# Kernel optimization log

Measured on AMD Instinct MI355X. Metric: run time of the kernel, lower is better.

The kernel has to match this reference:

```python
import jax, jax.numpy as jnp
import numpy as np

REG_COEF = 0.001


def setup_inputs() -> dict:
    key = jax.random.key(0)
    k1, k2, k3, k4 = jax.random.split(key, 4)
    B, K, d = 8192, 1024, 64
    q = jax.random.normal(k1, (B, d), dtype=jnp.float32)
    c = jax.random.normal(k2, (K, d), dtype=jnp.float32)
    # positive bandwidths, as produced by adjust_bandwidth (1/(2*rho^2))
    bandwidth = jax.random.uniform(k3, (K,), dtype=jnp.float32, minval=0.1, maxval=1.0)
    g_inv_c = jax.random.normal(k4, (K, d, d), dtype=jnp.float32)
    return {"q": q, "c": c, "bandwidth": bandwidth, "g_inv_c": g_inv_c}


def reference(q, c, bandwidth, g_inv_c):
    # squared euclidean distances: ||q-c||^2, computed via the expanded form
    sq_q = jnp.sum(q * q, axis=-1, keepdims=True)           # (B,1)
    sq_c = jnp.sum(c * c, axis=-1)                          # (K,)
    d2 = jnp.maximum(sq_q + sq_c[None, :] - 2.0 * (q @ c.T), 0.0)  # (B,K)
    weights = jnp.exp(-bandwidth[None, :] * d2)             # (B,K)
    g_inv = jnp.einsum('bk,kij->bij', weights, g_inv_c)     # (B,d,d)
    d = q.shape[-1]
    g_inv = g_inv + REG_COEF * jnp.eye(d, dtype=q.dtype)[None, :, :]
    return g_inv
```

## Files before the change

kernel.cpp:

```cpp
#include <hip/hip_runtime.h>
#include <hip/hip_bf16.h>

typedef __attribute__((ext_vector_type(8))) short bf16x8;
typedef __attribute__((ext_vector_type(4))) float f32x4;

#define Bsz 8192
#define Ksz 1024
#define Dsz 64
#define Nsz 4096

__device__ __forceinline__ void async_load16(const void* g, void* lds) {
    __builtin_amdgcn_global_load_lds(
        (const __attribute__((address_space(1))) void*)g,
        (__attribute__((address_space(3))) void*)lds,
        16, 0, 0);
}

__global__ __launch_bounds__(256) void transpose_convert(
    const float* __restrict__ G, __hip_bfloat16* __restrict__ Gt)
{
    __shared__ float tile[64][65];
    const int t = threadIdx.x;
    const int n0 = blockIdx.x * 64;
    const int k0 = blockIdx.y * 64;

    for (int i = 0; i < 4; ++i) {
        int f4 = t + 256 * i;
        int row = f4 >> 4;
        int c4  = (f4 & 15) << 2;
        float4 v = *(const float4*)&G[(size_t)(k0 + row) * Nsz + n0 + c4];
        tile[row][c4 + 0] = v.x;
        tile[row][c4 + 1] = v.y;
        tile[row][c4 + 2] = v.z;
        tile[row][c4 + 3] = v.w;
    }
    __syncthreads();
    for (int i = 0; i < 4; ++i) {
        int o = t + 256 * i;
        int rowp = o >> 4;
        int c4   = (o & 15) << 2;
        union { ushort4 u; __hip_bfloat16 h[4]; } cvt;
        cvt.h[0] = __float2bfloat16(tile[c4 + 0][rowp]);
        cvt.h[1] = __float2bfloat16(tile[c4 + 1][rowp]);
        cvt.h[2] = __float2bfloat16(tile[c4 + 2][rowp]);
        cvt.h[3] = __float2bfloat16(tile[c4 + 3][rowp]);
        *(ushort4*)&Gt[(size_t)(n0 + rowp) * Ksz + k0 + c4] = cvt.u;
    }
}

__global__ __launch_bounds__(256) void weights_kernel(
    const float* __restrict__ q, const float* __restrict__ c,
    const float* __restrict__ bw, __hip_bfloat16* __restrict__ W)
{
    __shared__ float qs[128][68];
    __shared__ float cs[128][68];
    __shared__ float sqq[128];
    __shared__ float sqc[128];

    const int t  = threadIdx.x;
    const int b0 = blockIdx.x * 128;
    const int k0 = blockIdx.y * 128;

    for (int i = 0; i < 8; ++i) {
        int f4 = t + 256 * i;
        int row = f4 >> 4;
        int c4  = (f4 & 15) << 2;
        float4 v = *(const float4*)&q[(size_t)(b0 + row) * Dsz + c4];
        qs[row][c4 + 0] = v.x; qs[row][c4 + 1] = v.y;
        qs[row][c4 + 2] = v.z; qs[row][c4 + 3] = v.w;
        float4 u = *(const float4*)&c[(size_t)(k0 + row) * Dsz + c4];
        cs[row][c4 + 0] = u.x; cs[row][c4 + 1] = u.y;
        cs[row][c4 + 2] = u.z; cs[row][c4 + 3] = u.w;
    }
    __syncthreads();

    if (t < 128) {
        float s = 0.f;
        for (int x = 0; x < 64; ++x) { float v = qs[t][x]; s += v * v; }
        sqq[t] = s;
    } else {
        int r = t - 128;
        float s = 0.f;
        for (int x = 0; x < 64; ++x) { float v = cs[r][x]; s += v * v; }
        sqc[r] = s;
    }
    __syncthreads();

    const int tx = t & 15;
    const int ty = t >> 4;

    float dot[8][8];
    for (int i = 0; i < 8; ++i)
        for (int j = 0; j < 8; ++j) dot[i][j] = 0.f;

    for (int x = 0; x < 64; ++x) {
        float qv[8], cv[8];
        #pragma unroll
        for (int i = 0; i < 8; ++i) qv[i] = qs[ty + 16 * i][x];
        #pragma unroll
        for (int j = 0; j < 8; ++j) cv[j] = cs[tx + 16 * j][x];
        #pragma unroll
        for (int i = 0; i < 8; ++i)
            #pragma unroll
            for (int j = 0; j < 8; ++j)
                dot[i][j] += qv[i] * cv[j];
    }

    for (int j = 0; j < 8; ++j) {
        int k = tx + 16 * j;
        float bwv = bw[k0 + k];
        float sc  = sqc[k];
        for (int i = 0; i < 8; ++i) {
            int b = ty + 16 * i;
            float d2 = fmaxf(sqq[b] + sc - 2.f * dot[i][j], 0.f);
            float w  = __expf(-bwv * d2);
            W[(size_t)(b0 + b) * Ksz + (k0 + k)] = __float2bfloat16(w);
        }
    }
}

#define TM 128
#define TN 128
#define BK 32

__global__ __launch_bounds__(256) void gemm_wg(
    const __hip_bfloat16* __restrict__ A,
    const __hip_bfloat16* __restrict__ Bt,
    float* __restrict__ C)
{
    __shared__ __attribute__((aligned(16))) __hip_bfloat16 As[TM * BK];
    __shared__ __attribute__((aligned(16))) __hip_bfloat16 Bs[TN * BK];

    const int t    = threadIdx.x;
    const int wave = t >> 6;
    const int lane = t & 63;
    const int m0 = blockIdx.y * TM;
    const int n0 = blockIdx.x * TN;

    const int wm = (wave >> 1) * 64;
    const int wn = (wave & 1) * 64;
    const int lrow = lane & 15;
    const int lk8  = (lane >> 4) << 3;

    f32x4 acc[4][4];
    for (int i = 0; i < 4; ++i)
        for (int j = 0; j < 4; ++j) acc[i][j] = (f32x4){0.f, 0.f, 0.f, 0.f};

    for (int k0 = 0; k0 < Ksz; k0 += BK) {
        __syncthreads();
        #pragma unroll
        for (int j = 0; j < 2; ++j) {
            int cb    = (wave * 2 + j) * 64;
            int chunk = cb + lane;
            int row   = chunk >> 2;
            int col8  = (chunk & 3) << 3;
            async_load16(A  + (size_t)(m0 + row) * Ksz + k0 + col8, &As[cb * 8]);
            async_load16(Bt + (size_t)(n0 + row) * Ksz + k0 + col8, &Bs[cb * 8]);
        }
        __syncthreads();

        bf16x8 af[4], bfr[4];
        #pragma unroll
        for (int i = 0; i < 4; ++i) {
            af[i]  = *(const bf16x8*)&As[(wm + i * 16 + lrow) * BK + lk8];
            bfr[i] = *(const bf16x8*)&Bs[(wn + i * 16 + lrow) * BK + lk8];
        }
        #pragma unroll
        for (int i = 0; i < 4; ++i)
            #pragma unroll
            for (int j = 0; j < 4; ++j)
                acc[i][j] = __builtin_amdgcn_mfma_f32_16x16x32_bf16(
                    af[i], bfr[j], acc[i][j], 0, 0, 0);
    }

    const int crow = (lane >> 4) << 2;
    const int ccol = lane & 15;
    for (int i = 0; i < 4; ++i) {
        for (int j = 0; j < 4; ++j) {
            int gn = n0 + wn + j * 16 + ccol;
            float diag = (gn % 65 == 0) ? 0.001f : 0.f;
            #pragma unroll
            for (int r = 0; r < 4; ++r) {
                int gm = m0 + wm + i * 16 + crow + r;
                C[(size_t)gm * Nsz + gn] = acc[i][j][r] + diag;
            }
        }
    }
}

extern "C" void kernel_launch(void* const* d_in, const int* in_sizes, int n_in,
                              void* d_out, int out_size, void* d_ws, size_t ws_size,
                              hipStream_t stream) {
    const float* q  = (const float*)d_in[0];
    const float* c  = (const float*)d_in[1];
    const float* bw = (const float*)d_in[2];
    const float* G  = (const float*)d_in[3];
    float* out = (float*)d_out;

    __hip_bfloat16* W  = (__hip_bfloat16*)d_ws;
    __hip_bfloat16* Gt = (__hip_bfloat16*)((char*)d_ws + (size_t)16 * 1024 * 1024);

    transpose_convert<<<dim3(Nsz / 64, Ksz / 64), 256, 0, stream>>>(G, Gt);
    weights_kernel<<<dim3(Bsz / 128, Ksz / 128), 256, 0, stream>>>(q, c, bw, W);
    gemm_wg<<<dim3(Nsz / TN, Bsz / TM), 256, 0, stream>>>(W, Gt, out);
}
```

Before: 233.3 us.

## Compute q·c distances with split-bf16 MFMA instead of scalar FP32 FMAs

Replaces the scalar FP32 outer-product loop in the weights kernel with bf16 MFMA instructions. q and 2c are each split into a high and a low bf16 part, and three MFMAs per tile (hh, hl, lh) recover close to FP32 accuracy for the dot product. Squared norms are rebuilt from the split parts. The aim is to move the distance GEMM onto matrix cores, at the cost of some precision loss in the exponent and extra LDS traffic from storing four bf16 arrays.

```diff
diff --git a/kernel.cpp b/kernel.cpp
--- a/kernel.cpp
+++ b/kernel.cpp
@@ -14,6 +14,12 @@
         (const __attribute__((address_space(1))) void*)g,
         (__attribute__((address_space(3))) void*)lds,
         16, 0, 0);
+}
+
+__device__ __forceinline__ float bf2f(unsigned short s) {
+    union { unsigned u; float f; } x;
+    x.u = ((unsigned)s) << 16;
+    return x.f;
 }
 
 __global__ __launch_bounds__(256) void transpose_convert(
@@ -48,12 +54,16 @@
     }
 }
 
-__global__ __launch_bounds__(256) void weights_kernel(
+#define QSTR 72
+
+__global__ __launch_bounds__(256) void weights_mfma(
     const float* __restrict__ q, const float* __restrict__ c,
     const float* __restrict__ bw, __hip_bfloat16* __restrict__ W)
 {
-    __shared__ float qs[128][68];
-    __shared__ float cs[128][68];
+    __shared__ __attribute__((aligned(16))) __hip_bfloat16 qh[128 * QSTR];
+    __shared__ __attribute__((aligned(16))) __hip_bfloat16 ql[128 * QSTR];
+    __shared__ __attribute__((aligned(16))) __hip_bfloat16 ch[128 * QSTR];
+    __shared__ __attribute__((aligned(16))) __hip_bfloat16 cl[128 * QSTR];
     __shared__ float sqq[128];
     __shared__ float sqc[128];
 
@@ -62,59 +72,105 @@
     const int k0 = blockIdx.y * 128;
 
     for (int i = 0; i < 8; ++i) {
-        int f4 = t + 256 * i;
+        int f4  = t + 256 * i;
         int row = f4 >> 4;
         int c4  = (f4 & 15) << 2;
         float4 v = *(const float4*)&q[(size_t)(b0 + row) * Dsz + c4];
-        qs[row][c4 + 0] = v.x; qs[row][c4 + 1] = v.y;
-        qs[row][c4 + 2] = v.z; qs[row][c4 + 3] = v.w;
         float4 u = *(const float4*)&c[(size_t)(k0 + row) * Dsz + c4];
-        cs[row][c4 + 0] = u.x; cs[row][c4 + 1] = u.y;
-        cs[row][c4 + 2] = u.z; cs[row][c4 + 3] = u.w;
+        float qv[4] = {v.x, v.y, v.z, v.w};
+        float cv[4] = {2.f * u.x, 2.f * u.y, 2.f * u.z, 2.f * u.w};
+        union { ushort4 u4; __hip_bfloat16 h[4]; } qhh, qll, chh, cll;
+        #pragma unroll
+        for (int e = 0; e < 4; ++e) {
+            __hip_bfloat16 hb = __float2bfloat16(qv[e]);
+            qhh.h[e] = hb;
+            qll.h[e] = __float2bfloat16(qv[e] - bf2f(*(unsigned short*)&hb));
+            __hip_bfloat16 hc = __float2bfloat16(cv[e]);
+            chh.h[e] = hc;
+            cll.h[e] = __float2bfloat16(cv[e] - bf2f(*(unsigned short*)&hc));
+        }
+        *(ushort4*)&qh[row * QSTR + c4] = qhh.u4;
+        *(ushort4*)&ql[row * QSTR + c4] = qll.u4;
+        *(ushort4*)&ch[row * QSTR + c4] = chh.u4;
+        *(ushort4*)&cl[row * QSTR + c4] = cll.u4;
     }
     __syncthreads();
 
     if (t < 128) {
         float s = 0.f;
-        for (int x = 0; x < 64; ++x) { float v = qs[t][x]; s += v * v; }
+        for (int x8 = 0; x8 < 64; x8 += 8) {
+            bf16x8 h = *(const bf16x8*)&qh[t * QSTR + x8];
+            bf16x8 l = *(const bf16x8*)&ql[t * QSTR + x8];
+            #pragma unroll
+            for (int e = 0; e < 8; ++e) {
+                float v = bf2f((unsigned short)h[e]) + bf2f((unsigned short)l[e]);
+                s += v * v;
+            }
+        }
         sqq[t] = s;
     } else {
         int r = t - 128;
         float s = 0.f;
-        for (int x = 0; x < 64; ++x) { float v = cs[r][x]; s += v * v; }
+        for (int x8 = 0; x8 < 64; x8 += 8) {
+            bf16x8 h = *(const bf16x8*)&ch[r * QSTR + x8];
+            bf16x8 l = *(const bf16x8*)&cl[r * QSTR + x8];
+            #pragma unroll
+            for (int e = 0; e < 8; ++e) {
+                float v = 0.5f * (bf2f((unsigned short)h[e]) + bf2f((unsigned short)l[e]));
+                s += v * v;
+            }
+        }
         sqc[r] = s;
     }
     __syncthreads();
 
-    const int tx = t & 15;
-    const int ty = t >> 4;
-
-    float dot[8][8];
-    for (int i = 0; i < 8; ++i)
-        for (int j = 0; j < 8; ++j) dot[i][j] = 0.f;
-
-    for (int x = 0; x < 64; ++x) {
-        float qv[8], cv[8];
-        #pragma unroll
-        for (int i = 0; i < 8; ++i) qv[i] = qs[ty + 16 * i][x];
-        #pragma unroll
-        for (int j = 0; j < 8; ++j) cv[j] = cs[tx + 16 * j][x];
-        #pragma unroll
-        for (int i = 0; i < 8; ++i)
-            #pragma unroll
-            for (int j = 0; j < 8; ++j)
-                dot[i][j] += qv[i] * cv[j];
-    }
-
-    for (int j = 0; j < 8; ++j) {
-        int k = tx + 16 * j;
+    const int wave = t >> 6;
+    const int lane = t & 63;
+    const int wm = (wave >> 1) * 64;
+    const int wn = (wave & 1) * 64;
+    const int lrow = lane & 15;
+    const int lk8  = (lane >> 4) << 3;
+
+    f32x4 acc[4][4];
+    for (int i = 0; i < 4; ++i)
+        for (int j = 0; j < 4; ++j) acc[i][j] = (f32x4){0.f, 0.f, 0.f, 0.f};
+
+    #pragma unroll
+    for (int ks = 0; ks < 64; ks += 32) {
+        bf16x8 ah[4], al[4], bh[4], bl[4];
+        #pragma unroll
+        for (int i = 0; i < 4; ++i) {
+            int ra = (wm + i * 16 + lrow) * QSTR + ks + lk8;
+            int rb = (wn + i * 16 + lrow) * QSTR + ks + lk8;
+            ah[i] = *(const bf16x8*)&qh[ra];
+            al[i] = *(const bf16x8*)&ql[ra];
+            bh[i] = *(const bf16x8*)&ch[rb];
+            bl[i] = *(const bf16x8*)&cl[rb];
+        }
+        #pragma unroll
+        for (int i = 0; i < 4; ++i)
+            #pragma unroll
+            for (int j = 0; j < 4; ++j) {
+                acc[i][j] = __builtin_amdgcn_mfma_f32_16x16x32_bf16(ah[i], bh[j], acc[i][j], 0, 0, 0);
+                acc[i][j] = __builtin_amdgcn_mfma_f32_16x16x32_bf16(ah[i], bl[j], acc[i][j], 0, 0, 0);
+                acc[i][j] = __builtin_amdgcn_mfma_f32_16x16x32_bf16(al[i], bh[j], acc[i][j], 0, 0, 0);
+            }
+    }
+
+    const int crow = (lane >> 4) << 2;
+    const int ccol = lane & 15;
+    for (int j = 0; j < 4; ++j) {
+        int k = wn + j * 16 + ccol;
         float bwv = bw[k0 + k];
         float sc  = sqc[k];
-        for (int i = 0; i < 8; ++i) {
-            int b = ty + 16 * i;
-            float d2 = fmaxf(sqq[b] + sc - 2.f * dot[i][j], 0.f);
-            float w  = __expf(-bwv * d2);
-            W[(size_t)(b0 + b) * Ksz + (k0 + k)] = __float2bfloat16(w);
+        #pragma unroll
+        for (int i = 0; i < 4; ++i) {
+            #pragma unroll
+            for (int r = 0; r < 4; ++r) {
+                int b = wm + i * 16 + crow + r;
+                float d2 = fmaxf(sqq[b] + sc - acc[i][j][r], 0.f);
+                W[(size_t)(b0 + b) * Ksz + (k0 + k)] = __float2bfloat16(__expf(-bwv * d2));
+            }
         }
     }
 }
@@ -201,6 +257,6 @@
     __hip_bfloat16* Gt = (__hip_bfloat16*)((char*)d_ws + (size_t)16 * 1024 * 1024);
 
     transpose_convert<<<dim3(Nsz / 64, Ksz / 64), 256, 0, stream>>>(G, Gt);
-    weights_kernel<<<dim3(Bsz / 128, Ksz / 128), 256, 0, stream>>>(q, c, bw, W);
+    weights_mfma<<<dim3(Bsz / 128, Ksz / 128), 256, 0, stream>>>(q, c, bw, W);
     gemm_wg<<<dim3(Nsz / TN, Bsz / TM), 256, 0, stream>>>(W, Gt, out);
 }
```

After: 227.5 us. 1.03x faster.
